# Kernel tuning notes

Hardware: AMD Instinct MI355X
Metric: run time of the kernel (lower is better)

Reference implementation:

```python
import math
import jax, jax.numpy as jnp
import numpy as np

D = 4096      # model dim
H = 32        # query heads
KVH = 8       # kv heads (GQA)
HD = D // H   # head dim = 128
B = 8         # batch == max_batch_size (cache returns full batch)
MAXLEN = 2048 # max_seq_len (cache length)
SEQ = 16      # new tokens this step
START = 1024  # start_pos (cache fill level)


def setup_inputs() -> dict:
    key = jax.random.key(0)
    ks = jax.random.split(key, 8)
    s = 0.02  # weight init scale
    x = jax.random.normal(ks[0], (B, SEQ, D), jnp.float32)
    wq = jax.random.normal(ks[1], (D, H * HD), jnp.float32) * s
    wk = jax.random.normal(ks[2], (D, KVH * HD), jnp.float32) * s
    wv = jax.random.normal(ks[3], (D, KVH * HD), jnp.float32) * s
    wo = jax.random.normal(ks[4], (H * HD, D), jnp.float32) * s
    # rotary tables: freqs_cis = exp(i * t * theta_j) -> (cos, sin)
    inv_freq = 1.0 / (10000.0 ** (jnp.arange(0, HD, 2, dtype=jnp.float32) / HD))  # [HD//2]
    ang = jnp.arange(MAXLEN, dtype=jnp.float32)[:, None] * inv_freq[None, :]      # [MAXLEN, HD//2]
    cos, sin = jnp.cos(ang), jnp.sin(ang)
    cache_k = jax.random.normal(ks[5], (B, MAXLEN, KVH, HD), jnp.float32)
    cache_v = jax.random.normal(ks[6], (B, MAXLEN, KVH, HD), jnp.float32)
    return dict(x=x, wq=wq, wk=wk, wv=wv, wo=wo, cos=cos, sin=sin,
                cache_k=cache_k, cache_v=cache_v, start_pos=START)


def _rotary(t, cos, sin):
    # t: [B,S,h,HD] viewed as complex pairs on last dim; cos/sin: [S, HD//2]
    tr = t.reshape(*t.shape[:-1], HD // 2, 2)
    t0, t1 = tr[..., 0], tr[..., 1]
    c = cos[None, :, None, :]
    s = sin[None, :, None, :]
    o0 = t0 * c - t1 * s
    o1 = t0 * s + t1 * c
    return jnp.stack([o0, o1], axis=-1).reshape(t.shape)


def reference(x, wq, wk, wv, wo, cos, sin, cache_k, cache_v, start_pos):
    bsz, seqlen, _ = x.shape
    q = (x @ wq).reshape(bsz, seqlen, H, HD)
    k = (x @ wk).reshape(bsz, seqlen, KVH, HD)
    v = (x @ wv).reshape(bsz, seqlen, KVH, HD)
    # rotary embedding on the current positions (fp32 like the original)
    cs = jax.lax.dynamic_slice_in_dim(cos, start_pos, seqlen, 0)
    sn = jax.lax.dynamic_slice_in_dim(sin, start_pos, seqlen, 0)
    q = _rotary(q.astype(jnp.float32), cs, sn).astype(x.dtype)
    k = _rotary(k.astype(jnp.float32), cs, sn).astype(x.dtype)
    # KV-cache update; attention runs over the full cache length
    keys = jax.lax.dynamic_update_slice(cache_k, k, (0, start_pos, 0, 0))
    vals = jax.lax.dynamic_update_slice(cache_v, v, (0, start_pos, 0, 0))
    # GQA repeat (tile-per-kv-head == jnp.repeat on head axis)
    n_rep = H // KVH
    keys = jnp.repeat(keys, n_rep, axis=2)  # [B, MAXLEN, H, HD]
    vals = jnp.repeat(vals, n_rep, axis=2)
    scores = jnp.einsum('bqhd,bkhd->bhqk', q, keys) / math.sqrt(HD)
    # pad mask from cache fill level (combine_masks with mask=None)
    valid = jnp.arange(keys.shape[1]) < start_pos + seqlen  # [MAXLEN]
    neg = jnp.asarray(-jnp.inf, scores.dtype)
    scores = jnp.where(valid[None, None, None, :], scores, neg)
    probs = jax.nn.softmax(scores.astype(jnp.float32), axis=-1).astype(q.dtype)
    out = jnp.einsum('bhqk,bkhd->bqhd', probs, vals).reshape(bsz, seqlen, H * HD)
    return out @ wo
```

## Files before the change

kernel.cpp:

```cpp
#include <hip/hip_runtime.h>
#include <math.h>
#include <stdint.h>

#define D 4096
#define H 32
#define KVH 8
#define HD 128
#define B_ 8
#define SEQ 16
#define MAXLEN 2048
#define NTOK 128
#define KSPLIT 8
#define KCH 512
#define BK 64
#define NSTEP (KCH / BK)
#define KSA 16

typedef __attribute__((ext_vector_type(8))) short bh8;
typedef __attribute__((ext_vector_type(4))) float f32x4;
typedef _Float16 f16x2 __attribute__((ext_vector_type(2)));
typedef _Float16 f16x8 __attribute__((ext_vector_type(8)));

static __device__ __forceinline__ int imin(int a, int b) { return a < b ? a : b; }

static __device__ __forceinline__ short f2bf(float x) {
    union { float f; uint32_t u; } v; v.f = x;
    uint32_t u = v.u;
    return (short)((u + 0x7fffu + ((u >> 16) & 1u)) >> 16);
}
static __device__ __forceinline__ float bf2f(short b) {
    union { uint32_t u; float f; } v; v.u = ((uint32_t)(uint16_t)b) << 16;
    return v.f;
}

static __device__ __forceinline__ float fexp2(float x) {
#if __has_builtin(__builtin_amdgcn_exp2f)
    return __builtin_amdgcn_exp2f(x);
#else
    return exp2f(x);
#endif
}

static __device__ __forceinline__ void gll16(const void* g, void* l) {
    __builtin_amdgcn_global_load_lds((const __attribute__((address_space(1))) uint32_t*)g,
                                     (__attribute__((address_space(3))) uint32_t*)l, 16, 0, 0);
}

__global__ __launch_bounds__(256) void cvt_x(const float* __restrict__ x, short* __restrict__ xp) {
    int i = blockIdx.x * 256 + threadIdx.x;
    int row = i >> 10;
    int c4 = (i & 1023) << 2;
    const float4 v = ((const float4*)x)[i];
    short4 o;
    o.x = f2bf(v.x); o.y = f2bf(v.y); o.z = f2bf(v.z); o.w = f2bf(v.w);
    *(short4*)&xp[((size_t)((c4 >> 3) * 128 + row)) * 8 + (c4 & 7)] = o;
}

__global__ __launch_bounds__(256) void gemm_mfma(const short* __restrict__ xp,
                                                 const float* __restrict__ wq,
                                                 const float* __restrict__ wk,
                                                 const float* __restrict__ wv,
                                                 short* __restrict__ Pq,
                                                 short* __restrict__ Pk,
                                                 short* __restrict__ Pv) {
    const int cbid = blockIdx.x;
    const int ks = blockIdx.y;
    const float* W; short* P; int ntot; int cb;
    if (cbid < 64)      { W = wq; P = Pq; ntot = 4096; cb = cbid * 64; }
    else if (cbid < 80) { W = wk; P = Pk; ntot = 1024; cb = (cbid - 64) * 64; }
    else                { W = wv; P = Pv; ntot = 1024; cb = (cbid - 80) * 64; }
    const int tid = threadIdx.x;
    const int lane = tid & 63;
    const int w = tid >> 6;
    const int wm = w >> 1, wn = w & 1;
    const int lrow = lane & 15, lkg = lane >> 4;
    const int k0 = ks * KCH;

    __shared__ short Asm[2][8 * 128 * 8];
    __shared__ short Wsm[2][8 * 64 * 8];

    f32x4 acc[4][2];
#pragma unroll
    for (int fm = 0; fm < 4; ++fm)
#pragma unroll
        for (int fn = 0; fn < 2; ++fn) acc[fm][fn] = (f32x4){0.f, 0.f, 0.f, 0.f};

    const int c2 = (tid & 31) * 2;
    const int kq = tid >> 5;
    const short* asrc = xp + ((size_t)(k0 >> 3)) * 1024;

    float2 wA[8], wB[8];
    auto loadW_A = [&](int t) {
        const float* p = W + (size_t)(k0 + t * BK + kq * 8) * ntot + cb + c2;
#pragma unroll
        for (int j = 0; j < 8; ++j) wA[j] = *(const float2*)(p + (size_t)j * ntot);
    };
    auto loadW_B = [&](int t) {
        const float* p = W + (size_t)(k0 + t * BK + kq * 8) * ntot + cb + c2;
#pragma unroll
        for (int j = 0; j < 8; ++j) wB[j] = *(const float2*)(p + (size_t)j * ntot);
    };
    auto loadA = [&](int t, int buf) {
        const short* ap = asrc + (size_t)t * 8192 + (size_t)tid * 8;
        short* ad = &Asm[buf][tid * 8];
        gll16(ap, ad);
        gll16(ap + 2048, ad + 2048);
        gll16(ap + 4096, ad + 4096);
        gll16(ap + 6144, ad + 6144);
    };
    auto writeW_A = [&](int buf) {
        bh8 w0, w1;
#pragma unroll
        for (int j = 0; j < 8; ++j) { w0[j] = f2bf(wA[j].x); w1[j] = f2bf(wA[j].y); }
        *(bh8*)&Wsm[buf][(size_t)(kq * 64 + c2) * 8] = w0;
        *(bh8*)&Wsm[buf][(size_t)(kq * 64 + c2 + 1) * 8] = w1;
    };
    auto writeW_B = [&](int buf) {
        bh8 w0, w1;
#pragma unroll
        for (int j = 0; j < 8; ++j) { w0[j] = f2bf(wB[j].x); w1[j] = f2bf(wB[j].y); }
        *(bh8*)&Wsm[buf][(size_t)(kq * 64 + c2) * 8] = w0;
        *(bh8*)&Wsm[buf][(size_t)(kq * 64 + c2 + 1) * 8] = w1;
    };
    auto compute = [&](int buf) {
#pragma unroll
        for (int h = 0; h < 2; ++h) {
            bh8 afr[4], bfr[2];
#pragma unroll
            for (int fn = 0; fn < 2; ++fn)
                bfr[fn] = *(const bh8*)&Wsm[buf][(size_t)((h * 4 + lkg) * 64 + wn * 32 + fn * 16 + lrow) * 8];
#pragma unroll
            for (int fm = 0; fm < 4; ++fm)
                afr[fm] = *(const bh8*)&Asm[buf][(size_t)((h * 4 + lkg) * 128 + wm * 64 + fm * 16 + lrow) * 8];
#pragma unroll
            for (int fm = 0; fm < 4; ++fm)
#pragma unroll
                for (int fn = 0; fn < 2; ++fn)
                    acc[fm][fn] = __builtin_amdgcn_mfma_f32_16x16x32_bf16(afr[fm], bfr[fn], acc[fm][fn], 0, 0, 0);
        }
    };

    loadA(0, 0);
    loadW_A(0);
    loadW_B(1);
    writeW_A(0);
    asm volatile("s_waitcnt vmcnt(8)" ::: "memory");
    __syncthreads();

    int buf = 0;
    for (int t = 0; t < NSTEP; ++t) {
        const bool haveN1 = (t + 1 < NSTEP), haveN2 = (t + 2 < NSTEP);
        if (haveN1) loadA(t + 1, buf ^ 1);
        if (haveN2) { if (t & 1) loadW_B(t + 2); else loadW_A(t + 2); }
        if (haveN1) { if (t & 1) writeW_A(buf ^ 1); else writeW_B(buf ^ 1); }
        compute(buf);
        if (haveN1) {
            if (haveN2) asm volatile("s_waitcnt vmcnt(8)" ::: "memory");
            else        asm volatile("s_waitcnt vmcnt(0)" ::: "memory");
        }
        __syncthreads();
        buf ^= 1;
    }

    short* pp = P + (size_t)ks * NTOK * ntot;
#pragma unroll
    for (int fm = 0; fm < 4; ++fm) {
        const int gr0 = wm * 64 + fm * 16 + lkg * 4;
#pragma unroll
        for (int fn = 0; fn < 2; ++fn) {
            const int gc = cb + wn * 32 + fn * 16 + lrow;
#pragma unroll
            for (int q = 0; q < 4; ++q)
                pp[(size_t)(gr0 + q) * ntot + gc] = f2bf(acc[fm][fn][q]);
        }
    }
}

__global__ __launch_bounds__(256) void combine_rot(const short* __restrict__ Pq,
                                                   const short* __restrict__ Pk,
                                                   const short* __restrict__ Pv,
                                                   float* __restrict__ qb,
                                                   float* __restrict__ knb,
                                                   float* __restrict__ vnb,
                                                   const float* __restrict__ cosT,
                                                   const float* __restrict__ sinT,
                                                   const int* __restrict__ startp) {
    int gid = blockIdx.x * 256 + threadIdx.x;
    int tok = gid / 3072;
    int pr = gid % 3072;
    int col = pr * 2;
    int start = *startp;
    int pos = start + (tok & (SEQ - 1));
    float a = 0.f, b = 0.f;
    if (col < 4096) {
        const short* base = Pq + (size_t)tok * 4096 + col;
#pragma unroll
        for (int ks = 0; ks < KSPLIT; ++ks) {
            short2 t = *(const short2*)(base + (size_t)ks * NTOK * 4096);
            a += bf2f(t.x); b += bf2f(t.y);
        }
        int i = (col & 127) >> 1;
        float c = cosT[pos * 64 + i], s = sinT[pos * 64 + i];
        qb[(size_t)tok * 4096 + col]     = a * c - b * s;
        qb[(size_t)tok * 4096 + col + 1] = a * s + b * c;
    } else if (col < 5120) {
        int colr = col - 4096;
        const short* base = Pk + (size_t)tok * 1024 + colr;
#pragma unroll
        for (int ks = 0; ks < KSPLIT; ++ks) {
            short2 t = *(const short2*)(base + (size_t)ks * NTOK * 1024);
            a += bf2f(t.x); b += bf2f(t.y);
        }
        int i = (colr & 127) >> 1;
        float c = cosT[pos * 64 + i], s = sinT[pos * 64 + i];
        knb[(size_t)tok * 1024 + colr]     = a * c - b * s;
        knb[(size_t)tok * 1024 + colr + 1] = a * s + b * c;
    } else {
        int colr = col - 5120;
        const short* base = Pv + (size_t)tok * 1024 + colr;
#pragma unroll
        for (int ks = 0; ks < KSPLIT; ++ks) {
            short2 t = *(const short2*)(base + (size_t)ks * NTOK * 1024);
            a += bf2f(t.x); b += bf2f(t.y);
        }
        vnb[(size_t)tok * 1024 + colr]     = a;
        vnb[(size_t)tok * 1024 + colr + 1] = b;
    }
}

__global__ __launch_bounds__(256) void attn_fused(const float* __restrict__ qb,
                                                  const float* __restrict__ knb,
                                                  const float* __restrict__ vnb,
                                                  const float* __restrict__ ck,
                                                  const float* __restrict__ cv,
                                                  short* __restrict__ Opart,
                                                  float* __restrict__ mpart,
                                                  float* __restrict__ lpart,
                                                  const int* __restrict__ startp) {
    const int ksb = blockIdx.x;
    const int kvh = blockIdx.y;
    const int b   = blockIdx.z;
    const int start = *startp;
    const int klen = start + SEQ;
    const int chunk = (klen + KSA - 1) / KSA;
    const int bbeg = ksb * chunk;
    const int bend = imin(bbeg + chunk, klen);
    const int tiles = (chunk + 31) >> 5;

    const int tid = threadIdx.x;
    const int w = tid >> 6, lane = tid & 63;
    const int c = lane & 15, g = lane >> 4;
    const int hh = kvh * 4 + w;

    __shared__ __align__(16) _Float16 Ksh[2][16][32][8];
    __shared__ __align__(16) _Float16 Vsh[2][4][128][8];

    const float scl2 = 0.08838834764831843f * 1.4426950408889634f;

    f16x8 qfr[4];
    {
        const float* qp = qb + (size_t)(b * SEQ + c) * 4096 + hh * 128 + 8 * g;
#pragma unroll
        for (int h = 0; h < 4; ++h) {
            float4 a = *(const float4*)(qp + 32 * h);
            float4 b2 = *(const float4*)(qp + 32 * h + 4);
            qfr[h][0] = (_Float16)(a.x * scl2);  qfr[h][1] = (_Float16)(a.y * scl2);
            qfr[h][2] = (_Float16)(a.z * scl2);  qfr[h][3] = (_Float16)(a.w * scl2);
            qfr[h][4] = (_Float16)(b2.x * scl2); qfr[h][5] = (_Float16)(b2.y * scl2);
            qfr[h][6] = (_Float16)(b2.z * scl2); qfr[h][7] = (_Float16)(b2.w * scl2);
        }
    }

    f32x4 acc_o[8];
#pragma unroll
    for (int dm = 0; dm < 8; ++dm) acc_o[dm] = (f32x4){0.f, 0.f, 0.f, 0.f};
    float mrun = -INFINITY, lrun = 0.f;

    const int s_   = tid & 31;
    const int dgA  = tid >> 5;
    const int koffK = 8 * ((s_ >> 2) & 3) + 4 * (s_ >> 4) + (s_ & 3);
    const int kg0 = tid >> 6, d0 = (tid & 63) * 2;

    float4 kr0, kr1, kr2, kr3;
    float2 vrw[8];
    auto gloadRaw = [&](int t) {
        const int kp = bbeg + t * 32 + koffK;
        kr0 = (float4){0.f,0.f,0.f,0.f}; kr1 = kr0; kr2 = kr0; kr3 = kr0;
        if (kp < bend) {
            const float* kr = (kp < start)
                ? ck + ((size_t)((b * MAXLEN + kp) * KVH + kvh)) * HD
                : knb + (size_t)(b * SEQ + kp - start) * 1024 + kvh * HD;
            kr0 = *(const float4*)(kr + dgA * 8);
            kr1 = *(const float4*)(kr + dgA * 8 + 4);
            kr2 = *(const float4*)(kr + dgA * 8 + 64);
            kr3 = *(const float4*)(kr + dgA * 8 + 68);
        }
#pragma unroll
        for (int j = 0; j < 8; ++j) {
            const int kpv = bbeg + t * 32 + kg0 * 8 + j;
            vrw[j] = (float2){0.f, 0.f};
            if (kpv < bend) {
                const float* vrp = (kpv < start)
                    ? cv + ((size_t)((b * MAXLEN + kpv) * KVH + kvh)) * HD + d0
                    : vnb + (size_t)(b * SEQ + kpv - start) * 1024 + kvh * HD + d0;
                vrw[j] = *(const float2*)vrp;
            }
        }
    };
    auto cvtStore = [&](int bf) {
        f16x8 ka, kb;
        ka[0]=(_Float16)kr0.x; ka[1]=(_Float16)kr0.y; ka[2]=(_Float16)kr0.z; ka[3]=(_Float16)kr0.w;
        ka[4]=(_Float16)kr1.x; ka[5]=(_Float16)kr1.y; ka[6]=(_Float16)kr1.z; ka[7]=(_Float16)kr1.w;
        kb[0]=(_Float16)kr2.x; kb[1]=(_Float16)kr2.y; kb[2]=(_Float16)kr2.z; kb[3]=(_Float16)kr2.w;
        kb[4]=(_Float16)kr3.x; kb[5]=(_Float16)kr3.y; kb[6]=(_Float16)kr3.z; kb[7]=(_Float16)kr3.w;
        *(f16x8*)&Ksh[bf][dgA][s_][0] = ka;
        *(f16x8*)&Ksh[bf][dgA + 8][s_][0] = kb;
        f16x8 w0, w1;
#pragma unroll
        for (int j = 0; j < 8; ++j) { w0[j] = (_Float16)vrw[j].x; w1[j] = (_Float16)vrw[j].y; }
        *(f16x8*)&Vsh[bf][kg0][d0][0] = w0;
        *(f16x8*)&Vsh[bf][kg0][d0 + 1][0] = w1;
    };

    gloadRaw(0);
    cvtStore(0);
    __syncthreads();

    int buf = 0;
    for (int t = 0; t < tiles; ++t) {
        if (t + 1 < tiles) gloadRaw(t + 1);
        const int nk = imin(32, bend - (bbeg + t * 32));

        f32x4 acc_s[2];
        acc_s[0] = (f32x4){0.f, 0.f, 0.f, 0.f};
        acc_s[1] = (f32x4){0.f, 0.f, 0.f, 0.f};
#pragma unroll
        for (int h = 0; h < 4; ++h) {
#pragma unroll
            for (int m = 0; m < 2; ++m) {
                const f16x8 afr = *(const f16x8*)&Ksh[buf][h * 4 + g][m * 16 + c][0];
                acc_s[m] = __builtin_amdgcn_mfma_f32_16x16x32_f16(afr, qfr[h], acc_s[m], 0, 0, 0);
            }
        }
        float s8[8];
#pragma unroll
        for (int m = 0; m < 2; ++m)
#pragma unroll
            for (int q = 0; q < 4; ++q) s8[m * 4 + q] = acc_s[m][q];
        if (nk < 32) {
#pragma unroll
            for (int jj = 0; jj < 8; ++jj)
                if (8 * g + jj >= nk) s8[jj] = -1e30f;
        }
        float tmax = s8[0];
#pragma unroll
        for (int jj = 1; jj < 8; ++jj) tmax = fmaxf(tmax, s8[jj]);
        tmax = fmaxf(tmax, __shfl_xor(tmax, 16));
        tmax = fmaxf(tmax, __shfl_xor(tmax, 32));
        if (__any(tmax > mrun + 11.5f)) {
            const float mn = fmaxf(mrun, tmax);
            const float fac = fexp2(mrun - mn);
            lrun *= fac;
#pragma unroll
            for (int dm = 0; dm < 8; ++dm) {
                acc_o[dm][0] *= fac; acc_o[dm][1] *= fac;
                acc_o[dm][2] *= fac; acc_o[dm][3] *= fac;
            }
            mrun = mn;
        }
        float pe[8];
#pragma unroll
        for (int jj = 0; jj < 8; ++jj) pe[jj] = fexp2(s8[jj] - mrun);
#pragma unroll
        for (int jj = 0; jj < 8; ++jj) lrun += pe[jj];
        f16x8 bp;
#pragma unroll
        for (int jj = 0; jj < 8; ++jj) bp[jj] = (_Float16)pe[jj];

#pragma unroll
        for (int dm = 0; dm < 8; ++dm) {
            const f16x8 av = *(const f16x8*)&Vsh[buf][g][dm * 16 + c][0];
            acc_o[dm] = __builtin_amdgcn_mfma_f32_16x16x32_f16(av, bp, acc_o[dm], 0, 0, 0);
        }

        if (t + 1 < tiles) cvtStore(buf ^ 1);
        __syncthreads();
        buf ^= 1;
    }

    lrun += __shfl_xor(lrun, 16);
    lrun += __shfl_xor(lrun, 32);

    const int base = ((b * KVH + kvh) * KSA + ksb) * 64;
    const int row = w * 16 + c;
#pragma unroll
    for (int dm = 0; dm < 8; ++dm) {
        short4 o4;
        o4.x = f2bf(acc_o[dm][0]); o4.y = f2bf(acc_o[dm][1]);
        o4.z = f2bf(acc_o[dm][2]); o4.w = f2bf(acc_o[dm][3]);
        *(short4*)&Opart[(size_t)(base + row) * 128 + dm * 16 + g * 4] = o4;
    }
    if (g == 0) { mpart[base + row] = mrun; lpart[base + row] = lrun; }
}

__global__ __launch_bounds__(256) void attn_merge(const short* __restrict__ Opart,
                                                  const float* __restrict__ mpart,
                                                  const float* __restrict__ lpart,
                                                  short* __restrict__ aob) {
    const int bkvh = blockIdx.x;
    const int tid = threadIdx.x;
    __shared__ float sf[KSA][64];
    __shared__ float sinvL[64];
    if (tid < 64) {
        const int row = tid;
        float M = -INFINITY;
#pragma unroll
        for (int ks = 0; ks < KSA; ++ks)
            M = fmaxf(M, mpart[(size_t)(bkvh * KSA + ks) * 64 + row]);
        float L = 0.f;
#pragma unroll
        for (int ks = 0; ks < KSA; ++ks) {
            float f = exp2f(mpart[(size_t)(bkvh * KSA + ks) * 64 + row] - M);
            sf[ks][row] = f;
            L += f * lpart[(size_t)(bkvh * KSA + ks) * 64 + row];
        }
        sinvL[row] = 1.f / L;
    }
    __syncthreads();
    const int b = bkvh >> 3, kvh = bkvh & 7;
    for (int e = tid; e < 2048; e += 256) {
        const int row = e >> 5;
        const int d4 = (e & 31) << 2;
        float a0 = 0.f, a1 = 0.f, a2 = 0.f, a3 = 0.f;
#pragma unroll
        for (int ks = 0; ks < KSA; ++ks) {
            const short4 sp = *(const short4*)&Opart[((size_t)(bkvh * KSA + ks) * 64 + row) * 128 + d4];
            const float f = sf[ks][row];
            a0 = fmaf(f, bf2f(sp.x), a0);
            a1 = fmaf(f, bf2f(sp.y), a1);
            a2 = fmaf(f, bf2f(sp.z), a2);
            a3 = fmaf(f, bf2f(sp.w), a3);
        }
        const float iL = sinvL[row];
        a0 *= iL; a1 *= iL; a2 *= iL; a3 *= iL;
        const int hh = kvh * 4 + (row >> 4);
        const int tok = b * SEQ + (row & 15);
        const int col = hh * 128 + d4;
        short4 o;
        o.x = f2bf(a0); o.y = f2bf(a1); o.z = f2bf(a2); o.w = f2bf(a3);
        *(short4*)&aob[((size_t)(col >> 3) * 128 + tok) * 8 + (col & 7)] = o;
    }
}

__global__ __launch_bounds__(256) void sum_parts(const short* __restrict__ P,
                                                 float* __restrict__ out) {
    int i = blockIdx.x * 256 + threadIdx.x;
    float a0 = 0.f, a1 = 0.f, a2 = 0.f, a3 = 0.f;
#pragma unroll
    for (int ks = 0; ks < KSPLIT; ++ks) {
        const short4 t = ((const short4*)(P + (size_t)ks * NTOK * 4096))[i];
        a0 += bf2f(t.x); a1 += bf2f(t.y); a2 += bf2f(t.z); a3 += bf2f(t.w);
    }
    ((float4*)out)[i] = make_float4(a0, a1, a2, a3);
}

extern "C" void kernel_launch(void* const* d_in, const int* in_sizes, int n_in,
                              void* d_out, int out_size, void* d_ws, size_t ws_size,
                              hipStream_t stream) {
    const float* x  = (const float*)d_in[0];
    const float* wq = (const float*)d_in[1];
    const float* wk = (const float*)d_in[2];
    const float* wv = (const float*)d_in[3];
    const float* wo = (const float*)d_in[4];
    const float* cs = (const float*)d_in[5];
    const float* sn = (const float*)d_in[6];
    const float* ck = (const float*)d_in[7];
    const float* cv = (const float*)d_in[8];
    const int* startp = (const int*)d_in[9];

    short* Opart = (short*)d_ws;
    short* Pqb = Opart;
    short* Pkb = Pqb + (size_t)KSPLIT * NTOK * 4096;
    short* Pvb = Pkb + (size_t)KSPLIT * NTOK * 1024;
    float* qb   = (float*)(Opart + (size_t)64 * KSA * 64 * 128);
    float* knb  = qb + (size_t)NTOK * 4096;
    float* vnb  = knb + (size_t)NTOK * 1024;
    short* xpre = (short*)(vnb + (size_t)NTOK * 1024);
    short* aob  = xpre + (size_t)NTOK * 4096;
    float* mpart = (float*)(aob + (size_t)NTOK * 4096);
    float* lpart = mpart + (size_t)64 * KSA * 64;

    cvt_x<<<512, 256, 0, stream>>>(x, xpre);
    gemm_mfma<<<dim3(96, KSPLIT), 256, 0, stream>>>(xpre, wq, wk, wv, Pqb, Pkb, Pvb);
    combine_rot<<<1536, 256, 0, stream>>>(Pqb, Pkb, Pvb, qb, knb, vnb, cs, sn, startp);
    attn_fused<<<dim3(KSA, KVH, B_), 256, 0, stream>>>(qb, knb, vnb, ck, cv, Opart, mpart, lpart, startp);
    attn_merge<<<64, 256, 0, stream>>>(Opart, mpart, lpart, aob);
    gemm_mfma<<<dim3(64, KSPLIT), 256, 0, stream>>>(aob, wo, wo, wo, Pqb, Pqb, Pqb);
    sum_parts<<<512, 256, 0, stream>>>(Pqb, (float*)d_out);
}
```

Measured before the change: 118.0 us.

## Widen GEMM tiles to 128 columns with 512-thread blocks and padded W layout

The projection GEMM now uses 512-thread blocks covering 128 output columns each, halving the grid. W is loaded as float4 and stored in LDS in a row-major layout padded to 68, replacing the k-group-interleaved layout. The two-deep register prefetch with explicit vmcnt waits becomes a simpler single-stage prefetch. This aims for wider, more coalesced weight loads and fewer blocks, at the cost of less latency hiding, fewer blocks across CUs, and split 8-byte LDS reads for B fragments.

```diff
diff --git a/kernel.cpp b/kernel.cpp
--- a/kernel.cpp
+++ b/kernel.cpp
@@ -56,19 +56,19 @@
     *(short4*)&xp[((size_t)((c4 >> 3) * 128 + row)) * 8 + (c4 & 7)] = o;
 }
 
-__global__ __launch_bounds__(256) void gemm_mfma(const short* __restrict__ xp,
-                                                 const float* __restrict__ wq,
-                                                 const float* __restrict__ wk,
-                                                 const float* __restrict__ wv,
-                                                 short* __restrict__ Pq,
-                                                 short* __restrict__ Pk,
-                                                 short* __restrict__ Pv) {
+__global__ __launch_bounds__(512, 4) void gemm_mfma(const short* __restrict__ xp,
+                                                    const float* __restrict__ wq,
+                                                    const float* __restrict__ wk,
+                                                    const float* __restrict__ wv,
+                                                    short* __restrict__ Pq,
+                                                    short* __restrict__ Pk,
+                                                    short* __restrict__ Pv) {
     const int cbid = blockIdx.x;
     const int ks = blockIdx.y;
     const float* W; short* P; int ntot; int cb;
-    if (cbid < 64)      { W = wq; P = Pq; ntot = 4096; cb = cbid * 64; }
-    else if (cbid < 80) { W = wk; P = Pk; ntot = 1024; cb = (cbid - 64) * 64; }
-    else                { W = wv; P = Pv; ntot = 1024; cb = (cbid - 80) * 64; }
+    if (cbid < 32)      { W = wq; P = Pq; ntot = 4096; cb = cbid * 128; }
+    else if (cbid < 40) { W = wk; P = Pk; ntot = 1024; cb = (cbid - 32) * 128; }
+    else                { W = wv; P = Pv; ntot = 1024; cb = (cbid - 40) * 128; }
     const int tid = threadIdx.x;
     const int lane = tid & 63;
     const int w = tid >> 6;
@@ -76,99 +76,82 @@
     const int lrow = lane & 15, lkg = lane >> 4;
     const int k0 = ks * KCH;
 
-    __shared__ short Asm[2][8 * 128 * 8];
-    __shared__ short Wsm[2][8 * 64 * 8];
-
-    f32x4 acc[4][2];
-#pragma unroll
-    for (int fm = 0; fm < 4; ++fm)
-#pragma unroll
-        for (int fn = 0; fn < 2; ++fn) acc[fm][fn] = (f32x4){0.f, 0.f, 0.f, 0.f};
-
-    const int c2 = (tid & 31) * 2;
+    __shared__ __align__(16) short Asm[2][8192];
+    __shared__ __align__(16) short Wsm[2][128 * 68];
+
+    f32x4 acc[2][4];
+#pragma unroll
+    for (int fm = 0; fm < 2; ++fm)
+#pragma unroll
+        for (int fn = 0; fn < 4; ++fn) acc[fm][fn] = (f32x4){0.f, 0.f, 0.f, 0.f};
+
+    const int c4 = (tid & 31) * 4;
     const int kq = tid >> 5;
-    const short* asrc = xp + ((size_t)(k0 >> 3)) * 1024;
-
-    float2 wA[8], wB[8];
-    auto loadW_A = [&](int t) {
-        const float* p = W + (size_t)(k0 + t * BK + kq * 8) * ntot + cb + c2;
-#pragma unroll
-        for (int j = 0; j < 8; ++j) wA[j] = *(const float2*)(p + (size_t)j * ntot);
-    };
-    auto loadW_B = [&](int t) {
-        const float* p = W + (size_t)(k0 + t * BK + kq * 8) * ntot + cb + c2;
-#pragma unroll
-        for (int j = 0; j < 8; ++j) wB[j] = *(const float2*)(p + (size_t)j * ntot);
-    };
-    auto loadA = [&](int t, int buf) {
-        const short* ap = asrc + (size_t)t * 8192 + (size_t)tid * 8;
-        short* ad = &Asm[buf][tid * 8];
+
+    float wrf[16];
+    auto loadW = [&](int t) {
+        const float* p = W + (size_t)(k0 + t * BK + kq * 4) * ntot + cb + c4;
+#pragma unroll
+        for (int j = 0; j < 4; ++j) *(float4*)&wrf[j * 4] = *(const float4*)(p + (size_t)j * ntot);
+    };
+    auto writeW = [&](int bufw) {
+#pragma unroll
+        for (int u = 0; u < 4; ++u) {
+            short4 o;
+            o.x = f2bf(wrf[0 * 4 + u]);
+            o.y = f2bf(wrf[1 * 4 + u]);
+            o.z = f2bf(wrf[2 * 4 + u]);
+            o.w = f2bf(wrf[3 * 4 + u]);
+            *(short4*)&Wsm[bufw][(c4 + u) * 68 + kq * 4] = o;
+        }
+    };
+    auto loadA = [&](int t, int bufa) {
+        const short* ap = xp + (size_t)(k0 >> 3) * 1024 + (size_t)t * 8192 + (size_t)tid * 8;
+        short* ad = &Asm[bufa][tid * 8];
         gll16(ap, ad);
-        gll16(ap + 2048, ad + 2048);
         gll16(ap + 4096, ad + 4096);
-        gll16(ap + 6144, ad + 6144);
-    };
-    auto writeW_A = [&](int buf) {
-        bh8 w0, w1;
-#pragma unroll
-        for (int j = 0; j < 8; ++j) { w0[j] = f2bf(wA[j].x); w1[j] = f2bf(wA[j].y); }
-        *(bh8*)&Wsm[buf][(size_t)(kq * 64 + c2) * 8] = w0;
-        *(bh8*)&Wsm[buf][(size_t)(kq * 64 + c2 + 1) * 8] = w1;
-    };
-    auto writeW_B = [&](int buf) {
-        bh8 w0, w1;
-#pragma unroll
-        for (int j = 0; j < 8; ++j) { w0[j] = f2bf(wB[j].x); w1[j] = f2bf(wB[j].y); }
-        *(bh8*)&Wsm[buf][(size_t)(kq * 64 + c2) * 8] = w0;
-        *(bh8*)&Wsm[buf][(size_t)(kq * 64 + c2 + 1) * 8] = w1;
-    };
-    auto compute = [&](int buf) {
+    };
+    auto compute = [&](int bufc) {
 #pragma unroll
         for (int h = 0; h < 2; ++h) {
-            bh8 afr[4], bfr[2];
-#pragma unroll
-            for (int fn = 0; fn < 2; ++fn)
-                bfr[fn] = *(const bh8*)&Wsm[buf][(size_t)((h * 4 + lkg) * 64 + wn * 32 + fn * 16 + lrow) * 8];
-#pragma unroll
-            for (int fm = 0; fm < 4; ++fm)
-                afr[fm] = *(const bh8*)&Asm[buf][(size_t)((h * 4 + lkg) * 128 + wm * 64 + fm * 16 + lrow) * 8];
-#pragma unroll
-            for (int fm = 0; fm < 4; ++fm)
-#pragma unroll
-                for (int fn = 0; fn < 2; ++fn)
-                    acc[fm][fn] = __builtin_amdgcn_mfma_f32_16x16x32_bf16(afr[fm], bfr[fn], acc[fm][fn], 0, 0, 0);
+            bh8 afr[2];
+#pragma unroll
+            for (int fm = 0; fm < 2; ++fm)
+                afr[fm] = *(const bh8*)&Asm[bufc][((h * 4 + lkg) * 128 + wm * 32 + fm * 16 + lrow) * 8];
+#pragma unroll
+            for (int fn = 0; fn < 4; ++fn) {
+                const short* bp = &Wsm[bufc][(wn * 64 + fn * 16 + lrow) * 68 + h * 32 + lkg * 8];
+                const short4 lo = *(const short4*)bp;
+                const short4 hi = *(const short4*)(bp + 4);
+                const bh8 bfr = (bh8){lo.x, lo.y, lo.z, lo.w, hi.x, hi.y, hi.z, hi.w};
+#pragma unroll
+                for (int fm = 0; fm < 2; ++fm)
+                    acc[fm][fn] = __builtin_amdgcn_mfma_f32_16x16x32_bf16(afr[fm], bfr, acc[fm][fn], 0, 0, 0);
+            }
         }
     };
 
     loadA(0, 0);
-    loadW_A(0);
-    loadW_B(1);
-    writeW_A(0);
-    asm volatile("s_waitcnt vmcnt(8)" ::: "memory");
+    loadW(0);
+    writeW(0);
     __syncthreads();
 
     int buf = 0;
     for (int t = 0; t < NSTEP; ++t) {
-        const bool haveN1 = (t + 1 < NSTEP), haveN2 = (t + 2 < NSTEP);
-        if (haveN1) loadA(t + 1, buf ^ 1);
-        if (haveN2) { if (t & 1) loadW_B(t + 2); else loadW_A(t + 2); }
-        if (haveN1) { if (t & 1) writeW_A(buf ^ 1); else writeW_B(buf ^ 1); }
+        if (t + 1 < NSTEP) { loadA(t + 1, buf ^ 1); loadW(t + 1); }
         compute(buf);
-        if (haveN1) {
-            if (haveN2) asm volatile("s_waitcnt vmcnt(8)" ::: "memory");
-            else        asm volatile("s_waitcnt vmcnt(0)" ::: "memory");
-        }
+        if (t + 1 < NSTEP) writeW(buf ^ 1);
         __syncthreads();
         buf ^= 1;
     }
 
     short* pp = P + (size_t)ks * NTOK * ntot;
 #pragma unroll
-    for (int fm = 0; fm < 4; ++fm) {
-        const int gr0 = wm * 64 + fm * 16 + lkg * 4;
-#pragma unroll
-        for (int fn = 0; fn < 2; ++fn) {
-            const int gc = cb + wn * 32 + fn * 16 + lrow;
+    for (int fm = 0; fm < 2; ++fm) {
+        const int gr0 = wm * 32 + fm * 16 + lkg * 4;
+#pragma unroll
+        for (int fn = 0; fn < 4; ++fn) {
+            const int gc = cb + wn * 64 + fn * 16 + lrow;
 #pragma unroll
             for (int q = 0; q < 4; ++q)
                 pp[(size_t)(gr0 + q) * ntot + gc] = f2bf(acc[fm][fn][q]);
@@ -491,10 +474,10 @@
     float* lpart = mpart + (size_t)64 * KSA * 64;
 
     cvt_x<<<512, 256, 0, stream>>>(x, xpre);
-    gemm_mfma<<<dim3(96, KSPLIT), 256, 0, stream>>>(xpre, wq, wk, wv, Pqb, Pkb, Pvb);
+    gemm_mfma<<<dim3(48, KSPLIT), 512, 0, stream>>>(xpre, wq, wk, wv, Pqb, Pkb, Pvb);
     combine_rot<<<1536, 256, 0, stream>>>(Pqb, Pkb, Pvb, qb, knb, vnb, cs, sn, startp);
     attn_fused<<<dim3(KSA, KVH, B_), 256, 0, stream>>>(qb, knb, vnb, ck, cv, Opart, mpart, lpart, startp);
     attn_merge<<<64, 256, 0, stream>>>(Opart, mpart, lpart, aob);
-    gemm_mfma<<<dim3(64, KSPLIT), 256, 0, stream>>>(aob, wo, wo, wo, Pqb, Pqb, Pqb);
+    gemm_mfma<<<dim3(32, KSPLIT), 512, 0, stream>>>(aob, wo, wo, wo, Pqb, Pqb, Pqb);
     sum_parts<<<512, 256, 0, stream>>>(Pqb, (float*)d_out);
 }
```

After: 110.5 us. -6.4%, faster.

## Load GEMM operands straight into registers and drop the LDS staging

Applied to the files above, without the earlier changes.

The QKV projection GEMM no longer stages the activation and weight tiles through double-buffered shared memory with barriers. Each wave now loads its own MFMA fragments directly from global memory into registers and software-pipelines two K-steps of 32. The aim is to remove LDS write and read traffic and the __syncthreads calls. The cost is that each weight element is fetched redundantly by the waves sharing a column tile, using scalar fp32 loads that are strided across rows.

```diff
diff --git a/kernel.cpp b/kernel.cpp
--- a/kernel.cpp
+++ b/kernel.cpp
@@ -12,8 +12,8 @@
 #define NTOK 128
 #define KSPLIT 8
 #define KCH 512
-#define BK 64
-#define NSTEP (KCH / BK)
+#define BK 32
+#define TSTEPS (KCH / BK)
 #define KSA 16
 
 typedef __attribute__((ext_vector_type(8))) short bh8;
@@ -39,11 +39,6 @@
 #else
     return exp2f(x);
 #endif
-}
-
-static __device__ __forceinline__ void gll16(const void* g, void* l) {
-    __builtin_amdgcn_global_load_lds((const __attribute__((address_space(1))) uint32_t*)g,
-                                     (__attribute__((address_space(3))) uint32_t*)l, 16, 0, 0);
 }
 
 __global__ __launch_bounds__(256) void cvt_x(const float* __restrict__ x, short* __restrict__ xp) {
@@ -76,90 +71,49 @@
     const int lrow = lane & 15, lkg = lane >> 4;
     const int k0 = ks * KCH;
 
-    __shared__ short Asm[2][8 * 128 * 8];
-    __shared__ short Wsm[2][8 * 64 * 8];
-
     f32x4 acc[4][2];
 #pragma unroll
     for (int fm = 0; fm < 4; ++fm)
 #pragma unroll
         for (int fn = 0; fn < 2; ++fn) acc[fm][fn] = (f32x4){0.f, 0.f, 0.f, 0.f};
 
-    const int c2 = (tid & 31) * 2;
-    const int kq = tid >> 5;
-    const short* asrc = xp + ((size_t)(k0 >> 3)) * 1024;
-
-    float2 wA[8], wB[8];
-    auto loadW_A = [&](int t) {
-        const float* p = W + (size_t)(k0 + t * BK + kq * 8) * ntot + cb + c2;
-#pragma unroll
-        for (int j = 0; j < 8; ++j) wA[j] = *(const float2*)(p + (size_t)j * ntot);
+    const short* abase = xp + ((size_t)((k0 >> 3) + lkg) * 128 + wm * 64 + lrow) * 8;
+    const float* wbase = W + (size_t)(k0 + lkg * 8) * ntot + cb + wn * 32 + lrow;
+
+    auto loadWf = [&](int t, float (&wr)[16]) {
+        const float* p = wbase + (size_t)t * 32 * ntot;
+#pragma unroll
+        for (int j = 0; j < 8; ++j) {
+            wr[j]     = p[0];
+            wr[8 + j] = p[16];
+            p += ntot;
+        }
     };
-    auto loadW_B = [&](int t) {
-        const float* p = W + (size_t)(k0 + t * BK + kq * 8) * ntot + cb + c2;
-#pragma unroll
-        for (int j = 0; j < 8; ++j) wB[j] = *(const float2*)(p + (size_t)j * ntot);
+    auto loadAf = [&](int t, bh8 (&ar)[4]) {
+        const short* p = abase + (size_t)t * 4096;
+#pragma unroll
+        for (int fm = 0; fm < 4; ++fm)
+            ar[fm] = *(const bh8*)(p + fm * 128);
     };
-    auto loadA = [&](int t, int buf) {
-        const short* ap = asrc + (size_t)t * 8192 + (size_t)tid * 8;
-        short* ad = &Asm[buf][tid * 8];
-        gll16(ap, ad);
-        gll16(ap + 2048, ad + 2048);
-        gll16(ap + 4096, ad + 4096);
-        gll16(ap + 6144, ad + 6144);
+    auto comp = [&](const bh8 (&ar)[4], const float (&wr)[16]) {
+        bh8 bf0, bf1;
+#pragma unroll
+        for (int j = 0; j < 8; ++j) { bf0[j] = f2bf(wr[j]); bf1[j] = f2bf(wr[8 + j]); }
+#pragma unroll
+        for (int fm = 0; fm < 4; ++fm) {
+            acc[fm][0] = __builtin_amdgcn_mfma_f32_16x16x32_bf16(ar[fm], bf0, acc[fm][0], 0, 0, 0);
+            acc[fm][1] = __builtin_amdgcn_mfma_f32_16x16x32_bf16(ar[fm], bf1, acc[fm][1], 0, 0, 0);
+        }
     };
-    auto writeW_A = [&](int buf) {
-        bh8 w0, w1;
-#pragma unroll
-        for (int j = 0; j < 8; ++j) { w0[j] = f2bf(wA[j].x); w1[j] = f2bf(wA[j].y); }
-        *(bh8*)&Wsm[buf][(size_t)(kq * 64 + c2) * 8] = w0;
-        *(bh8*)&Wsm[buf][(size_t)(kq * 64 + c2 + 1) * 8] = w1;
-    };
-    auto writeW_B = [&](int buf) {
-        bh8 w0, w1;
-#pragma unroll
-        for (int j = 0; j < 8; ++j) { w0[j] = f2bf(wB[j].x); w1[j] = f2bf(wB[j].y); }
-        *(bh8*)&Wsm[buf][(size_t)(kq * 64 + c2) * 8] = w0;
-        *(bh8*)&Wsm[buf][(size_t)(kq * 64 + c2 + 1) * 8] = w1;
-    };
-    auto compute = [&](int buf) {
-#pragma unroll
-        for (int h = 0; h < 2; ++h) {
-            bh8 afr[4], bfr[2];
-#pragma unroll
-            for (int fn = 0; fn < 2; ++fn)
-                bfr[fn] = *(const bh8*)&Wsm[buf][(size_t)((h * 4 + lkg) * 64 + wn * 32 + fn * 16 + lrow) * 8];
-#pragma unroll
-            for (int fm = 0; fm < 4; ++fm)
-                afr[fm] = *(const bh8*)&Asm[buf][(size_t)((h * 4 + lkg) * 128 + wm * 64 + fm * 16 + lrow) * 8];
-#pragma unroll
-            for (int fm = 0; fm < 4; ++fm)
-#pragma unroll
-                for (int fn = 0; fn < 2; ++fn)
-                    acc[fm][fn] = __builtin_amdgcn_mfma_f32_16x16x32_bf16(afr[fm], bfr[fn], acc[fm][fn], 0, 0, 0);
-        }
-    };
-
-    loadA(0, 0);
-    loadW_A(0);
-    loadW_B(1);
-    writeW_A(0);
-    asm volatile("s_waitcnt vmcnt(8)" ::: "memory");
-    __syncthreads();
-
-    int buf = 0;
-    for (int t = 0; t < NSTEP; ++t) {
-        const bool haveN1 = (t + 1 < NSTEP), haveN2 = (t + 2 < NSTEP);
-        if (haveN1) loadA(t + 1, buf ^ 1);
-        if (haveN2) { if (t & 1) loadW_B(t + 2); else loadW_A(t + 2); }
-        if (haveN1) { if (t & 1) writeW_A(buf ^ 1); else writeW_B(buf ^ 1); }
-        compute(buf);
-        if (haveN1) {
-            if (haveN2) asm volatile("s_waitcnt vmcnt(8)" ::: "memory");
-            else        asm volatile("s_waitcnt vmcnt(0)" ::: "memory");
-        }
-        __syncthreads();
-        buf ^= 1;
+
+    float wr0[16], wr1[16];
+    bh8 ar0[4], ar1[4];
+    loadWf(0, wr0); loadAf(0, ar0);
+    for (int t = 0; t < TSTEPS; t += 2) {
+        loadWf(t + 1, wr1); loadAf(t + 1, ar1);
+        comp(ar0, wr0);
+        if (t + 2 < TSTEPS) { loadWf(t + 2, wr0); loadAf(t + 2, ar0); }
+        comp(ar1, wr1);
     }
 
     short* pp = P + (size_t)ks * NTOK * ntot;
```

Measured after the change: 106.1 us. 1.11x faster.
